# Optimization experiments

Hardware: AMD Instinct MI355X
Metric: run time of the kernel (lower is better)

## Reference

```python
import jax, jax.numpy as jnp
import numpy as np
from jax import lax

B, C, H, L = 4, 64, 8, 2048  # batch, per-head channels, heads, sequence length


def setup_inputs() -> dict:
    key = jax.random.key(0)
    ks = jax.random.split(key, 15)

    def p(k, shape, s=0.05):
        return jax.random.normal(k, shape, jnp.float32) * s

    inp = {"x": jax.random.normal(ks[0], (B, C, L), jnp.float32)}
    for i, nm in enumerate(["q", "k", "v"]):
        inp[f"{nm}_dw"] = p(ks[1 + 4 * i], (C, 1, 3))       # depthwise conv weight, groups=C, k=3
        inp[f"{nm}_db"] = p(ks[2 + 4 * i], (C,))
        inp[f"{nm}_pw"] = p(ks[3 + 4 * i], (H * C, C))      # pointwise 1x1 conv weight
        inp[f"{nm}_pb"] = p(ks[4 + 4 * i], (H * C,))
    inp["u_w"] = p(ks[13], (C, H * C))                      # unify_heads 1x1 conv weight
    inp["u_b"] = p(ks[14], (C,))
    return inp


def dsconv(x, dw, db, pw, pb):
    # Depth-separable conv1d: depthwise (k=3, pad=1, groups=C) then pointwise 1x1.
    c = x.shape[1]
    y = lax.conv_general_dilated(x, dw, window_strides=(1,), padding=[(1, 1)],
                                 dimension_numbers=("NCH", "OIH", "NCH"),
                                 feature_group_count=c)
    y = y + db[None, :, None]
    return jnp.einsum("bcl,oc->bol", y, pw) + pb[None, :, None]


def reference(x, q_dw, q_db, q_pw, q_pb, k_dw, k_db, k_pw, k_pb,
              v_dw, v_db, v_pw, v_pb, u_w, u_b):
    b, c, l = x.shape
    h = H
    scale = c ** (-0.25)
    q = dsconv(x, q_dw, q_db, q_pw, q_pb).reshape(b, h, c, l) * scale
    k = dsconv(x, k_dw, k_db, k_pw, k_pb).reshape(b, h, c, l) * scale
    v = dsconv(x, v_dw, v_db, v_pw, v_pb).reshape(b, h, c, l)
    # dot[b,h,i,j] = sum_c k[b,h,c,i] * q[b,h,c,j]  (i = key pos, j = query pos)
    dot = jnp.einsum("bhci,bhcj->bhij", k, q)
    att = jax.nn.softmax(dot, axis=2)  # normalize over key positions (torch dim=1 of [bh,l,l])
    out = jnp.einsum("bhci,bhij->bhcj", v, att).reshape(b, h * c, l)
    return jnp.einsum("bkl,ck->bcl", out, u_w) + u_b[None, :, None]
```

## Files before the change

kernel.cpp:

```cpp
#include <hip/hip_runtime.h>
#include <hip/hip_bf16.h>
#include <stdint.h>
#include <string.h>

typedef unsigned short u16;
typedef unsigned int u32;
typedef __bf16 bf16x8 __attribute__((ext_vector_type(8)));
typedef float f32x4 __attribute__((ext_vector_type(4)));

#define NB 4
#define NC 64
#define NH 8
#define NL 2048
#define HC 512

#define XT_OFF  ((size_t)0)
#define WM_OFF  ((size_t)1 << 20)
#define PBM_OFF ((size_t)2 << 20)
#define V_OFF   ((size_t)4 << 20)
#define QT_OFF  ((size_t)12 << 20)
#define KT_OFF  ((size_t)20 << 20)

#define LP 68

#if __has_builtin(__builtin_amdgcn_exp2f)
#define EXP2F __builtin_amdgcn_exp2f
#else
#define EXP2F exp2f
#endif

static __device__ __forceinline__ u16 f2bfu(float f) {
  union { float f; unsigned int i; } x; x.f = f;
  unsigned int i = x.i;
  return (u16)((i + 0x7fffu + ((i >> 16) & 1u)) >> 16);
}
static __device__ __forceinline__ u32 pk2(float a, float b) {
  float2 f; f.x = a; f.y = b;
  __hip_bfloat162 h = __float22bfloat162_rn(f);
  u32 w; __builtin_memcpy(&w, &h, 4); return w;
}
static __device__ __forceinline__ bf16x8 ld_bf8(const u16* p) {
  bf16x8 v; __builtin_memcpy(&v, p, 16); return v;
}

__global__ __launch_bounds__(256) void prep_all(
    const float* __restrict__ x,
    const float* __restrict__ qdw, const float* __restrict__ qdb,
    const float* __restrict__ qpw, const float* __restrict__ qpb,
    const float* __restrict__ kdw, const float* __restrict__ kdb,
    const float* __restrict__ kpw, const float* __restrict__ kpb,
    const float* __restrict__ vdw, const float* __restrict__ vdb,
    const float* __restrict__ vpw, const float* __restrict__ vpb,
    const float* __restrict__ ub,
    u16* __restrict__ Wm, float* __restrict__ pbm,
    u16* __restrict__ xT, float* __restrict__ out)
{
  __shared__ __align__(16) u16 T[64 * LP];
  int bx = blockIdx.x;
  int tid = threadIdx.x;

  if (bx < 512) {
    int i4 = bx * 256 + tid;
    int c = (i4 >> 9) & 63;
    float f = ub[c];
    float4 v = {f, f, f, f};
    ((float4*)out)[i4] = v;
    return;
  }
  if (bx < 902) {
    int idx = (bx - 512) * 256 + tid;
    if (idx < 98304) {
      int tns = idx >> 15, r = idx & 32767, o = r >> 6, c = r & 63;
      const float* dw = (tns == 0) ? qdw : (tns == 1) ? kdw : vdw;
      const float* pw = (tns == 0) ? qpw : (tns == 1) ? kpw : vpw;
      float s = (tns == 0) ? 0.35355339059327373f * 1.4426950408889634f
              : (tns == 1) ? 0.35355339059327373f : 1.0f;
      float w = pw[o * 64 + c] * s;
#pragma unroll
      for (int d = 0; d < 3; ++d)
        Wm[((size_t)(tns * 3 + d) * 512 + o) * 64 + c] = f2bfu(w * dw[c * 3 + d]);
    } else {
      int i = idx - 98304;
      int tns = i >> 9, o = i & 511;
      const float* db = (tns == 0) ? qdb : (tns == 1) ? kdb : vdb;
      const float* pw = (tns == 0) ? qpw : (tns == 1) ? kpw : vpw;
      const float* pb = (tns == 0) ? qpb : (tns == 1) ? kpb : vpb;
      float s = (tns == 0) ? 0.35355339059327373f * 1.4426950408889634f
              : (tns == 1) ? 0.35355339059327373f : 1.0f;
      float bias = pb[o];
      for (int c = 0; c < 64; ++c) bias += pw[o * 64 + c] * db[c];
      pbm[i] = bias * s;
    }
    return;
  }
  {
    int b2 = bx - 902;
    int lt = b2 & 31, b = b2 >> 5;
    {
      int c = tid & 63, ls = (tid >> 6) * 16;
      const float4* g = (const float4*)(x + ((size_t)b * NC + c) * NL + lt * 64 + ls);
      u16 tmp[16];
#pragma unroll
      for (int j4 = 0; j4 < 4; ++j4) {
        float4 f = g[j4];
        tmp[j4*4+0] = f2bfu(f.x); tmp[j4*4+1] = f2bfu(f.y);
        tmp[j4*4+2] = f2bfu(f.z); tmp[j4*4+3] = f2bfu(f.w);
      }
#pragma unroll
      for (int j = 0; j < 16; ++j) T[(ls + j) * LP + c] = tmp[j];
    }
    __syncthreads();
    {
      int r = tid >> 2, cs = (tid & 3) * 16;
      uint4 a = *(const uint4*)&T[r * LP + cs];
      uint4 b3 = *(const uint4*)&T[r * LP + cs + 8];
      u16* o = xT + ((size_t)b * NL + lt * 64 + r) * 64 + cs;
      *(uint4*)o = a;
      *(uint4*)(o + 8) = b3;
    }
  }
}

__global__ __launch_bounds__(256) void qkv_gemm(
    const u16* __restrict__ xT, const u16* __restrict__ Wm,
    const float* __restrict__ pbm,
    u16* __restrict__ v, u16* __restrict__ qT, u16* __restrict__ kT)
{
  __shared__ __align__(16) u16 WS[3][64 * LP];
  __shared__ __align__(16) u16 XS[2][66 * LP];
  __shared__ __align__(16) u16 OS[64 * LP];

  int bx = blockIdx.x;
  int lg  = bx & 7;
  int och = (bx >> 3) & 7;
  int tmp = bx >> 6;
  int tns = tmp % 3;
  int b   = tmp / 3;

  int tid = threadIdx.x;
  int wave = tid >> 6, lane = tid & 63, quad = lane >> 4, l16 = lane & 15;
  const u16* xg = xT + (size_t)b * NL * 64;

  {
    const u16* wg = Wm + ((size_t)(tns * 3) * 512 + och * 64) * 64;
#pragma unroll
    for (int it = 0; it < 6; ++it) {
      int s = tid + it * 256;
      int d = s >> 9, r = s & 511;
      int o = r >> 3, c4 = r & 7;
      uint4 w = *(const uint4*)(wg + ((size_t)d * 512 + o) * 64 + c4 * 8);
      *(uint4*)&WS[d][o * LP + c4 * 8] = w;
    }
  }

  int xr0 = tid >> 3,          xc0 = (tid & 7) * 8;
  int xr1 = (tid + 256) >> 3,  xc1 = xc0;
  int xr2 = (tid + 512) >> 3,  xc2 = xc0;
  uint4 R0, R1, R2;
  uint4 Z = {0, 0, 0, 0};

#define LOAD_XS(tt)                                                         \
  {                                                                         \
    int base = (lg * 4 + (tt)) * 64 - 1;                                    \
    int g0 = base + xr0, g1 = base + xr1, g2 = base + xr2;                  \
    R0 = ((unsigned)g0 < NL) ? *(const uint4*)(xg + (size_t)g0 * 64 + xc0) : Z; \
    R1 = ((unsigned)g1 < NL) ? *(const uint4*)(xg + (size_t)g1 * 64 + xc1) : Z; \
    if (tid < 16)                                                           \
      R2 = ((unsigned)g2 < NL) ? *(const uint4*)(xg + (size_t)g2 * 64 + xc2) : Z; \
  }
#define STORE_XS(bf)                                                        \
  {                                                                         \
    *(uint4*)&XS[bf][xr0 * LP + xc0] = R0;                                  \
    *(uint4*)&XS[bf][xr1 * LP + xc1] = R1;                                  \
    if (tid < 16) *(uint4*)&XS[bf][xr2 * LP + xc2] = R2;                    \
  }

  LOAD_XS(0); STORE_XS(0);
  LOAD_XS(1);
  __syncthreads();

  float bias4[4];
  bf16x8 aw[3][2];
  if (tns == 2) {
    const float* pbt = pbm + tns * 512 + och * 64 + wave * 16;
#pragma unroll
    for (int rr = 0; rr < 4; ++rr) bias4[rr] = pbt[quad * 4 + rr];
#pragma unroll
    for (int d = 0; d < 3; ++d)
#pragma unroll
      for (int kh = 0; kh < 2; ++kh)
        aw[d][kh] = ld_bf8(&WS[d][(wave * 16 + l16) * LP + kh * 32 + quad * 8]);
  } else {
    const float* pbt = pbm + tns * 512 + och * 64;
#pragma unroll
    for (int nt = 0; nt < 4; ++nt) bias4[nt] = pbt[nt * 16 + l16];
  }

  for (int t = 0; t < 4; ++t) {
    int cur = t & 1;
    f32x4 acc[4] = {{0,0,0,0},{0,0,0,0},{0,0,0,0},{0,0,0,0}};

    if (tns == 2) {
#pragma unroll
      for (int nt = 0; nt < 4; ++nt)
#pragma unroll
        for (int d = 0; d < 3; ++d)
#pragma unroll
          for (int kh = 0; kh < 2; ++kh) {
            bf16x8 bx8 = ld_bf8(&XS[cur][(nt * 16 + l16 + d) * LP + kh * 32 + quad * 8]);
            acc[nt] = __builtin_amdgcn_mfma_f32_16x16x32_bf16(aw[d][kh], bx8, acc[nt], 0, 0, 0);
          }
    } else {
      bf16x8 ax[3][2];
#pragma unroll
      for (int d = 0; d < 3; ++d)
#pragma unroll
        for (int kh = 0; kh < 2; ++kh)
          ax[d][kh] = ld_bf8(&XS[cur][(wave * 16 + l16 + d) * LP + kh * 32 + quad * 8]);
#pragma unroll
      for (int nt = 0; nt < 4; ++nt)
#pragma unroll
        for (int d = 0; d < 3; ++d)
#pragma unroll
          for (int kh = 0; kh < 2; ++kh) {
            bf16x8 bw = ld_bf8(&WS[d][(nt * 16 + l16) * LP + kh * 32 + quad * 8]);
            acc[nt] = __builtin_amdgcn_mfma_f32_16x16x32_bf16(ax[d][kh], bw, acc[nt], 0, 0, 0);
          }
    }

    if (t < 3) { STORE_XS((t + 1) & 1); if (t < 2) LOAD_XS(t + 2); }
    __syncthreads();

    if (tns == 2) {
#pragma unroll
      for (int nt = 0; nt < 4; ++nt)
#pragma unroll
        for (int rr = 0; rr < 4; ++rr)
          OS[(wave * 16 + quad * 4 + rr) * LP + nt * 16 + l16] =
              f2bfu(acc[nt][rr] + bias4[rr]);
    } else {
#pragma unroll
      for (int nt = 0; nt < 4; ++nt)
#pragma unroll
        for (int rr = 0; rr < 4; ++rr)
          OS[(wave * 16 + quad * 4 + rr) * LP + nt * 16 + l16] =
              f2bfu(acc[nt][rr] + bias4[nt]);
    }

    {
      int lt = lg * 4 + t;
      int r = wave * 16 + (lane >> 2), ck = (lane & 3) * 16;
      uint4 a = *(const uint4*)&OS[r * LP + ck];
      uint4 b2 = *(const uint4*)&OS[r * LP + ck + 8];
      u16* gp;
      if (tns == 2)
        gp = v + ((size_t)(b * HC + och * 64 + r)) * NL + lt * 64 + ck;
      else {
        u16* dst = (tns == 0) ? qT : kT;
        gp = dst + ((size_t)(b * 8 + och) * NL + lt * 64 + r) * 64 + ck;
      }
      *(uint4*)gp = a;
      *(uint4*)(gp + 8) = b2;
    }
  }
#undef LOAD_XS
#undef STORE_XS
}

__global__ __launch_bounds__(256) void attn_kernel(
    const u16* __restrict__ qT, const u16* __restrict__ kT,
    const u16* __restrict__ vg, const float* __restrict__ uw,
    float* __restrict__ outg)
{
  __shared__ __align__(16) u16 Kt[64 * LP];
  __shared__ __align__(16) u16 Vt[64 * LP];
  __shared__ __align__(16) u16 UW[64 * LP];
  __shared__ __align__(16) u16 PB[4][16 * LP];

  int bx = blockIdx.x;
  int bh = bx & 31, qt = bx >> 5;
  int b = bh >> 3, h = bh & 7;
  int tid = threadIdx.x;
  int wave = tid >> 6, lane = tid & 63, quad = lane >> 4, l16 = lane & 15;

  const u16* Qh = qT + (size_t)bh * NL * 64;
  const u16* Kh = kT + (size_t)bh * NL * 64;
  const u16* Vh = vg + ((size_t)(b * HC + h * NC)) * NL;
  int q0 = qt * 128;

  int sr = tid >> 2, ss = (tid & 3) * 16;
  int vc = tid & 63, vk = (tid >> 6) * 16;

  {
    int c = tid >> 2, g = (tid & 3) * 16;
    const float4* s = (const float4*)(uw + (size_t)c * HC + h * 64 + g);
#pragma unroll
    for (int j = 0; j < 4; ++j) {
      float4 w = s[j];
      u16* d = &UW[c * LP + g + j * 4];
      d[0] = f2bfu(w.x); d[1] = f2bfu(w.y); d[2] = f2bfu(w.z); d[3] = f2bfu(w.w);
    }
  }

  bf16x8 bq[2][2];
#pragma unroll
  for (int t = 0; t < 2; ++t)
#pragma unroll
    for (int kh = 0; kh < 2; ++kh)
      bq[t][kh] = ld_bf8(Qh + (size_t)(q0 + wave * 32 + t * 16 + l16) * 64
                         + kh * 32 + quad * 8);

  f32x4 o[2][4];
#pragma unroll
  for (int t = 0; t < 2; ++t)
#pragma unroll
    for (int ct = 0; ct < 4; ++ct) o[t][ct] = (f32x4){0, 0, 0, 0};
  float l_part[2] = {0.f, 0.f};

  uint4 ka, kb, va, vb;
  {
    const u16* ks = Kh + (size_t)sr * 64 + ss;
    ka = *(const uint4*)ks; kb = *(const uint4*)(ks + 8);
    const u16* vs = Vh + (size_t)vc * NL + vk;
    va = *(const uint4*)vs; vb = *(const uint4*)(vs + 8);
  }
  __syncthreads();

  u16* Pw = &PB[wave][0];

  for (int i = 0; i < 32; ++i) {
    *(uint4*)&Kt[sr * LP + ss] = ka;
    *(uint4*)&Kt[sr * LP + ss + 8] = kb;
    *(uint4*)&Vt[vc * LP + vk] = va;
    *(uint4*)&Vt[vc * LP + vk + 8] = vb;
    __syncthreads();
    if (i < 31) {
      int kt1 = (i + 1) * 64;
      const u16* ks = Kh + (size_t)(kt1 + sr) * 64 + ss;
      ka = *(const uint4*)ks; kb = *(const uint4*)(ks + 8);
      const u16* vs = Vh + (size_t)vc * NL + kt1 + vk;
      va = *(const uint4*)vs; vb = *(const uint4*)(vs + 8);
    }

    bf16x8 ak[4][2], av[4][2];
#pragma unroll
    for (int j = 0; j < 4; ++j)
#pragma unroll
      for (int kh = 0; kh < 2; ++kh) {
        ak[j][kh] = ld_bf8(&Kt[(j * 16 + l16) * LP + kh * 32 + quad * 8]);
        av[j][kh] = ld_bf8(&Vt[(j * 16 + l16) * LP + kh * 32 + quad * 8]);
      }

#pragma unroll
    for (int t = 0; t < 2; ++t) {
      f32x4 s[4];
#pragma unroll
      for (int ktl = 0; ktl < 4; ++ktl) {
        f32x4 z = {0, 0, 0, 0};
        z = __builtin_amdgcn_mfma_f32_16x16x32_bf16(ak[ktl][0], bq[t][0], z, 0, 0, 0);
        z = __builtin_amdgcn_mfma_f32_16x16x32_bf16(ak[ktl][1], bq[t][1], z, 0, 0, 0);
        s[ktl] = z;
      }
      u16* Pq = &Pw[l16 * LP];
#pragma unroll
      for (int ktl = 0; ktl < 4; ++ktl) {
        float p0 = EXP2F(s[ktl][0]);
        float p1 = EXP2F(s[ktl][1]);
        float p2 = EXP2F(s[ktl][2]);
        float p3 = EXP2F(s[ktl][3]);
        l_part[t] += p0 + p1 + p2 + p3;
        *(u32*)&Pq[ktl * 16 + quad * 4] = pk2(p0, p1);
        *(u32*)&Pq[ktl * 16 + quad * 4 + 2] = pk2(p2, p3);
      }
#pragma unroll
      for (int kh = 0; kh < 2; ++kh) {
        bf16x8 bp = ld_bf8(&Pq[kh * 32 + quad * 8]);
#pragma unroll
        for (int ct = 0; ct < 4; ++ct)
          o[t][ct] = __builtin_amdgcn_mfma_f32_16x16x32_bf16(av[ct][kh], bp, o[t][ct], 0, 0, 0);
      }
    }
    __syncthreads();
  }

  float* ob = outg + ((size_t)b * NC) * NL;
#pragma unroll
  for (int t = 0; t < 2; ++t) {
    float lp = l_part[t];
    lp += __shfl_xor(lp, 16);
    lp += __shfl_xor(lp, 32);
    float rinv = 1.0f / lp;
    u16* OT = &Pw[l16 * LP];
    *(u32*)&OT[ 0 + quad * 4]     = pk2(o[t][0][0]*rinv, o[t][0][1]*rinv);
    *(u32*)&OT[ 0 + quad * 4 + 2] = pk2(o[t][0][2]*rinv, o[t][0][3]*rinv);
    *(u32*)&OT[16 + quad * 4]     = pk2(o[t][1][0]*rinv, o[t][1][1]*rinv);
    *(u32*)&OT[16 + quad * 4 + 2] = pk2(o[t][1][2]*rinv, o[t][1][3]*rinv);
    *(u32*)&OT[32 + quad * 4]     = pk2(o[t][2][0]*rinv, o[t][2][1]*rinv);
    *(u32*)&OT[32 + quad * 4 + 2] = pk2(o[t][2][2]*rinv, o[t][2][3]*rinv);
    *(u32*)&OT[48 + quad * 4]     = pk2(o[t][3][0]*rinv, o[t][3][1]*rinv);
    *(u32*)&OT[48 + quad * 4 + 2] = pk2(o[t][3][2]*rinv, o[t][3][3]*rinv);

    int qcol = q0 + wave * 32 + t * 16 + l16;
#pragma unroll
    for (int mt = 0; mt < 4; ++mt) {
      f32x4 acc = {0, 0, 0, 0};
#pragma unroll
      for (int kh = 0; kh < 2; ++kh) {
        bf16x8 a = ld_bf8(&UW[(mt * 16 + l16) * LP + kh * 32 + quad * 8]);
        bf16x8 bt = ld_bf8(&OT[kh * 32 + quad * 8]);
        acc = __builtin_amdgcn_mfma_f32_16x16x32_bf16(a, bt, acc, 0, 0, 0);
      }
#pragma unroll
      for (int rr = 0; rr < 4; ++rr) {
        int c = mt * 16 + quad * 4 + rr;
        atomicAdd(&ob[(size_t)c * NL + qcol], acc[rr]);
      }
    }
  }
}

extern "C" void kernel_launch(void* const* d_in, const int* in_sizes, int n_in,
                              void* d_out, int out_size, void* d_ws, size_t ws_size,
                              hipStream_t stream) {
  (void)in_sizes; (void)n_in; (void)out_size; (void)ws_size;
  const float* x   = (const float*)d_in[0];
  const float* qdw = (const float*)d_in[1];
  const float* qdb = (const float*)d_in[2];
  const float* qpw = (const float*)d_in[3];
  const float* qpb = (const float*)d_in[4];
  const float* kdw = (const float*)d_in[5];
  const float* kdb = (const float*)d_in[6];
  const float* kpw = (const float*)d_in[7];
  const float* kpb = (const float*)d_in[8];
  const float* vdw = (const float*)d_in[9];
  const float* vdb = (const float*)d_in[10];
  const float* vpw = (const float*)d_in[11];
  const float* vpb = (const float*)d_in[12];
  const float* uw  = (const float*)d_in[13];
  const float* ub  = (const float*)d_in[14];

  char* ws = (char*)d_ws;
  u16*   xT  = (u16*)(ws + XT_OFF);
  u16*   Wm  = (u16*)(ws + WM_OFF);
  float* pbm = (float*)(ws + PBM_OFF);
  u16*   v   = (u16*)(ws + V_OFF);
  u16*   qT  = (u16*)(ws + QT_OFF);
  u16*   kT  = (u16*)(ws + KT_OFF);
  float* out = (float*)d_out;

  prep_all<<<1030, 256, 0, stream>>>(
      x, qdw, qdb, qpw, qpb, kdw, kdb, kpw, kpb, vdw, vdb, vpw, vpb,
      ub, Wm, pbm, xT, out);
  qkv_gemm<<<768, 256, 0, stream>>>(xT, Wm, pbm, v, qT, kT);
  attn_kernel<<<512, 256, 0, stream>>>(qT, kT, v, uw, out);
}
```

Measured before the change: 164.3 us.

## Load K/V MFMA fragments directly from global memory instead of via LDS

Removes the shared-memory staging of K and V tiles and the per-iteration block barriers in the attention loop; each wave now reads its MFMA operand fragments straight from global memory (relying on L1/L2 for reuse across the 4 waves). This eliminates LDS writes, reads and two __syncthreads per iteration and lowers LDS usage, which may raise occupancy. The cost is 4x redundant global/cache traffic for K/V and the loss of the register prefetch that overlapped the next tile's load with compute, so load latency is now exposed directly before the MFMAs.

```diff
diff --git a/kernel.cpp b/kernel.cpp
--- a/kernel.cpp
+++ b/kernel.cpp
@@ -272,8 +272,6 @@
     const u16* __restrict__ vg, const float* __restrict__ uw,
     float* __restrict__ outg)
 {
-  __shared__ __align__(16) u16 Kt[64 * LP];
-  __shared__ __align__(16) u16 Vt[64 * LP];
   __shared__ __align__(16) u16 UW[64 * LP];
   __shared__ __align__(16) u16 PB[4][16 * LP];
 
@@ -288,9 +286,6 @@
   const u16* Vh = vg + ((size_t)(b * HC + h * NC)) * NL;
   int q0 = qt * 128;
 
-  int sr = tid >> 2, ss = (tid & 3) * 16;
-  int vc = tid & 63, vk = (tid >> 6) * 16;
-
   {
     int c = tid >> 2, g = (tid & 3) * 16;
     const float4* s = (const float4*)(uw + (size_t)c * HC + h * 64 + g);
@@ -317,38 +312,22 @@
     for (int ct = 0; ct < 4; ++ct) o[t][ct] = (f32x4){0, 0, 0, 0};
   float l_part[2] = {0.f, 0.f};
 
-  uint4 ka, kb, va, vb;
-  {
-    const u16* ks = Kh + (size_t)sr * 64 + ss;
-    ka = *(const uint4*)ks; kb = *(const uint4*)(ks + 8);
-    const u16* vs = Vh + (size_t)vc * NL + vk;
-    va = *(const uint4*)vs; vb = *(const uint4*)(vs + 8);
-  }
   __syncthreads();
 
   u16* Pw = &PB[wave][0];
 
   for (int i = 0; i < 32; ++i) {
-    *(uint4*)&Kt[sr * LP + ss] = ka;
-    *(uint4*)&Kt[sr * LP + ss + 8] = kb;
-    *(uint4*)&Vt[vc * LP + vk] = va;
-    *(uint4*)&Vt[vc * LP + vk + 8] = vb;
-    __syncthreads();
-    if (i < 31) {
-      int kt1 = (i + 1) * 64;
-      const u16* ks = Kh + (size_t)(kt1 + sr) * 64 + ss;
-      ka = *(const uint4*)ks; kb = *(const uint4*)(ks + 8);
-      const u16* vs = Vh + (size_t)vc * NL + kt1 + vk;
-      va = *(const uint4*)vs; vb = *(const uint4*)(vs + 8);
-    }
+    int kt0 = i * 64;
 
     bf16x8 ak[4][2], av[4][2];
 #pragma unroll
     for (int j = 0; j < 4; ++j)
 #pragma unroll
       for (int kh = 0; kh < 2; ++kh) {
-        ak[j][kh] = ld_bf8(&Kt[(j * 16 + l16) * LP + kh * 32 + quad * 8]);
-        av[j][kh] = ld_bf8(&Vt[(j * 16 + l16) * LP + kh * 32 + quad * 8]);
+        ak[j][kh] = ld_bf8(Kh + (size_t)(kt0 + j * 16 + l16) * 64
+                           + kh * 32 + quad * 8);
+        av[j][kh] = ld_bf8(Vh + (size_t)(j * 16 + l16) * NL + kt0
+                           + kh * 32 + quad * 8);
       }
 
 #pragma unroll
@@ -380,7 +359,6 @@
           o[t][ct] = __builtin_amdgcn_mfma_f32_16x16x32_bf16(av[ct][kh], bp, o[t][ct], 0, 0, 0);
       }
     }
-    __syncthreads();
   }
 
   float* ob = outg + ((size_t)b * NC) * NL;
```

Measured after the change: 230.0 us. 1.4x slower.
